# Kernel tuning notes

Hardware: AMD Instinct MI355X
Metric: run time of the kernel (lower is better)

The kernel has to match this reference:

```python
import jax, jax.numpy as jnp
import numpy as np

T, D, H, P, HEADS, EC = 16, 192, 128, 128, 4, 32  # EC = proj_dim // 4
HD = P // HEADS  # head dim = 32


def setup_inputs() -> dict:
    key = jax.random.key(0)
    ks = jax.random.split(key, 16)
    def nrm(k, shp, s=0.02):
        return jax.random.normal(k, shp, jnp.float32) * s
    x = jax.random.normal(ks[0], (T, H, D), jnp.float32)
    u = jax.random.uniform(ks[1], (D, D))
    w = jax.random.uniform(ks[2], (D, D))
    edge_w = jnp.where(u < 0.05, w, 0.0)
    return dict(
        x=x, edge_w=edge_w,
        W_node=nrm(ks[3], (H, P)), b_node=jnp.zeros(P),
        W_edge=nrm(ks[4], (1, EC)), b_edge=jnp.zeros(EC),
        time_enc=nrm(ks[5], (P,)),
        Wqkv=nrm(ks[6], (P, 3 * P)), bqkv=jnp.zeros(3 * P),
        Wo=nrm(ks[7], (P, P)), bo=jnp.zeros(P),
        W1=nrm(ks[8], (P, 4 * P)), b1=jnp.zeros(4 * P),
        W2=nrm(ks[9], (4 * P, P)), b2=jnp.zeros(P),
        g1=jnp.ones(P), beta1=jnp.zeros(P), g2=jnp.ones(P), beta2=jnp.zeros(P),
        Wc1=nrm(ks[10], (2 * P + EC, P)), bc1=jnp.zeros(P),
        Wc2=nrm(ks[11], (P, 1)), bc2=jnp.zeros(1),
        Wd1=nrm(ks[12], (2 * P, P)), bd1=jnp.zeros(P),
        Wd2=nrm(ks[13], (P, 1)), bd2=jnp.zeros(1),
    )


def _ln(z, g, b):
    m = z.mean(-1, keepdims=True)
    v = ((z - m) ** 2).mean(-1, keepdims=True)
    return (z - m) / jnp.sqrt(v + 1e-5) * g + b


def _heads(t, S):
    return t.reshape(S, HEADS, HD).transpose(1, 0, 2)  # (h, S, hd)


def _forward(x, edge_w, W_node, b_node, W_edge, b_edge, time_enc, Wqkv, bqkv,
             Wo, bo, W1, b1, W2, b2, g1, beta1, g2, beta2,
             Wc1, bc1, Wc2, bc2, Wd1, bd1, Wd2, bd2):
    S = T * D
    # node encoder: (T,H,D) -> (T,D,H) -> (T*D,H) -> (T*D,P), dropout is eval-mode identity
    xf = x.transpose(0, 2, 1).reshape(S, H)
    h = jax.nn.relu(xf @ W_node + b_node)
    # learned time encoding scaled by time index
    t_idx = jnp.repeat(jnp.arange(T, dtype=jnp.float32), D)
    h = h + time_enc[None, :] * t_idx[:, None]
    # spatiotemporal mask: attend to self+neighbors at t and t-1 (vectorized kron)
    adj = (edge_w > 0) | jnp.eye(D, dtype=bool)
    time_allow = jnp.eye(T, dtype=bool) | jnp.eye(T, k=-1, dtype=bool)
    allow = (time_allow[:, None, :, None] & adj[None, :, None, :]).reshape(S, S)
    scale = 1.0 / np.sqrt(HD)
    z = h
    for _ in range(2):  # num_layers=2, shared weights as in the source
        y = _ln(z, g1, beta1)
        qkv = y @ Wqkv + bqkv
        q, k, v = jnp.split(qkv, 3, axis=-1)
        scores = jnp.einsum('hqd,hkd->hqk', _heads(q, S), _heads(k, S)) * scale
        scores = jnp.where(allow[None], scores, -jnp.inf)
        a = jax.nn.softmax(scores, axis=-1)
        attn = jnp.einsum('hqk,hkd->hqd', a, _heads(v, S))
        z = z + attn.transpose(1, 0, 2).reshape(S, P) @ Wo + bo
        y = _ln(z, g2, beta2)
        z = z + jax.nn.relu(y @ W1 + b1) @ W2 + b2
    nf = z.reshape(T, D, P)
    curr, nxt = nf[:-1], nf[1:]  # (T-1, D, P)
    # edge encoder: Linear(1->EC)+ReLU on edge weights
    edge_enc = jax.nn.relu(edge_w[:, :, None] * W_edge[0] + b_edge)  # (D, D, EC)
    # update classifier on concat[next_i, curr_j, edge] -> split the first matmul
    hn = nxt @ Wc1[:P]            # (T-1, D, P)
    hc = curr @ Wc1[P:2 * P]      # (T-1, D, P)
    he = edge_enc @ Wc1[2 * P:]   # (D, D, P)
    hcls = jax.nn.relu(hn[:, :, None, :] + hc[:, None, :, :] + he[None] + bc1)
    logits = (hcls @ Wc2)[..., 0] + bc2[0]  # (T-1, D, D)
    mask = (edge_w == 0) & ~jnp.eye(D, dtype=bool)
    logits = jnp.where(mask[None], -1e9, logits)
    # distance predictor on concat[curr, next]
    hd = jax.nn.relu(curr @ Wd1[:P] + nxt @ Wd1[P:] + bd1)
    dist = (hd @ Wd2)[..., 0] + bd2[0]  # (T-1, D)
    return logits, dist


def reference(x, edge_w, W_node, b_node, W_edge, b_edge, time_enc, Wqkv, bqkv,
              Wo, bo, W1, b1, W2, b2, g1, beta1, g2, beta2,
              Wc1, bc1, Wc2, bc2, Wd1, bd1, Wd2, bd2):
    return _forward(x, edge_w, W_node, b_node, W_edge, b_edge, time_enc, Wqkv,
                    bqkv, Wo, bo, W1, b1, W2, b2, g1, beta1, g2, beta2,
                    Wc1, bc1, Wc2, bc2, Wd1, bd1, Wd2, bd2)
```

## Files before the change

kernel.cpp:

```cpp
#include <hip/hip_runtime.h>

constexpr int T_ = 16;
constexpr int D_ = 192;
constexpr int H_ = 128;
constexpr int P_ = 128;
constexpr int EC_ = 32;
constexpr int S_ = T_ * D_;
constexpr int FF_ = 512;
constexpr float SCALE_ = 0.17677669529663687f;

__device__ __forceinline__ float wave_sum64(float v) {
#pragma unroll
  for (int m = 1; m < 64; m <<= 1) v += __shfl_xor(v, m);
  return v;
}

__global__ __launch_bounds__(128) void embed_adj_kernel(
    const float* __restrict__ x, const float* __restrict__ W_node,
    const float* __restrict__ b_node, const float* __restrict__ time_enc,
    const float* __restrict__ edge_w, float* __restrict__ z,
    int* __restrict__ adj_cnt, int* __restrict__ adj_list) {
  int bx = blockIdx.x;
  int tid = threadIdx.x;
  if (bx < D_ && tid < 64) {
    int lane = tid, cnt = 0;
    for (int base = 0; base < D_; base += 64) {
      int j = base + lane;
      bool pred = (edge_w[bx * D_ + j] > 0.f) || (j == bx);
      unsigned long long mb = __ballot(pred);
      int ofs = __popcll(mb & ((1ull << lane) - 1ull));
      if (pred) adj_list[bx * D_ + cnt + ofs] = j;
      cnt += __popcll(mb);
    }
    if (lane == 0) adj_cnt[bx] = cnt;
  }
  __shared__ float As[4 * H_];
  int m0 = bx * 4;
  for (int idx = tid; idx < 4 * H_; idx += 128) {
    int r = idx >> 7, h = idx & 127;
    int s = m0 + r, t = s / D_, d = s - t * D_;
    As[idx] = x[(t * H_ + h) * D_ + d];
  }
  __syncthreads();
  int j = tid;
  float acc[4];
  float bj = b_node[j];
#pragma unroll
  for (int r = 0; r < 4; ++r) acc[r] = bj;
  for (int h = 0; h < H_; h += 4) {
    float w0 = W_node[(h + 0) * P_ + j], w1 = W_node[(h + 1) * P_ + j];
    float w2 = W_node[(h + 2) * P_ + j], w3 = W_node[(h + 3) * P_ + j];
#pragma unroll
    for (int r = 0; r < 4; ++r) {
      const float4 a = *reinterpret_cast<const float4*>(&As[r * H_ + h]);
      acc[r] = fmaf(a.x, w0, acc[r]);
      acc[r] = fmaf(a.y, w1, acc[r]);
      acc[r] = fmaf(a.z, w2, acc[r]);
      acc[r] = fmaf(a.w, w3, acc[r]);
    }
  }
  float te = time_enc[j];
#pragma unroll
  for (int r = 0; r < 4; ++r) {
    int s = m0 + r;
    z[(size_t)s * P_ + j] = fmaxf(acc[r], 0.f) + te * (float)(s / D_);
  }
}

__global__ __launch_bounds__(384) void qkv_kernel(
    const float* __restrict__ z, const float* __restrict__ Wqkv,
    const float* __restrict__ bqkv, const float* __restrict__ g,
    const float* __restrict__ b, float* __restrict__ qkvb) {
  constexpr int BM = 4, N = 384;
  int m0 = blockIdx.x * BM;
  int tid = threadIdx.x;
  __shared__ float As[BM * 128];
  {
    float4* As4 = (float4*)As;
    const float4* Z4 = (const float4*)(z + (size_t)m0 * 128);
    if (tid < BM * 32) As4[tid] = Z4[tid];
  }
  __syncthreads();
  {
    int wv = tid >> 6, lane = tid & 63;
    if (wv < BM) {
      int r = wv;
      float v0 = As[r * 128 + lane], v1 = As[r * 128 + 64 + lane];
      float s = wave_sum64(v0 + v1);
      float mean = s * (1.f / 128.f);
      float d0 = v0 - mean, d1 = v1 - mean;
      float q = wave_sum64(d0 * d0 + d1 * d1);
      float inv = 1.f / sqrtf(q * (1.f / 128.f) + 1e-5f);
      As[r * 128 + lane] = d0 * inv * g[lane] + b[lane];
      As[r * 128 + 64 + lane] = d1 * inv * g[lane + 64] + b[lane + 64];
    }
  }
  __syncthreads();
  int col = tid;
  float acc[BM];
  float bc = bqkv[col];
#pragma unroll
  for (int r = 0; r < BM; ++r) acc[r] = bc;
  for (int k = 0; k < 128; k += 4) {
    float b0 = Wqkv[(size_t)(k + 0) * N + col];
    float b1 = Wqkv[(size_t)(k + 1) * N + col];
    float b2 = Wqkv[(size_t)(k + 2) * N + col];
    float b3 = Wqkv[(size_t)(k + 3) * N + col];
#pragma unroll
    for (int r = 0; r < BM; ++r) {
      const float4 a = *(const float4*)&As[r * 128 + k];
      acc[r] = fmaf(a.x, b0, acc[r]);
      acc[r] = fmaf(a.y, b1, acc[r]);
      acc[r] = fmaf(a.z, b2, acc[r]);
      acc[r] = fmaf(a.w, b3, acc[r]);
    }
  }
#pragma unroll
  for (int r = 0; r < BM; ++r) qkvb[(size_t)(m0 + r) * N + col] = acc[r];
}

__global__ __launch_bounds__(128) void attn_wo_kernel(
    const float* __restrict__ qkvb, const int* __restrict__ adj_cnt,
    const int* __restrict__ adj_list, const float* __restrict__ Wo,
    const float* __restrict__ bo, float* __restrict__ z) {
  int s = blockIdx.x;
  int t = s / D_, d1 = s - t * D_;
  int tid = threadIdx.x;
  __shared__ int klist[D_];
  __shared__ float scores[4][2 * D_];
  __shared__ float att[128];

  int nd2 = adj_cnt[d1];
  for (int kd = tid; kd < nd2; kd += 128) klist[kd] = adj_list[d1 * D_ + kd];
  __syncthreads();
  int t0 = (t > 0) ? t - 1 : 0;
  int ntp = (t > 0) ? 2 : 1;
  int nk = nd2 * ntp;

  float q = qkvb[(size_t)s * 384 + tid];
  int h = tid >> 5, dd = tid & 31;

  for (int tp = 0; tp < ntp; ++tp) {
    int tt = t0 + tp;
    int kd = 0;
    for (; kd + 2 <= nd2; kd += 2) {
      int sk0 = tt * D_ + klist[kd];
      int sk1 = tt * D_ + klist[kd + 1];
      float p0 = q * qkvb[(size_t)sk0 * 384 + P_ + tid];
      float p1 = q * qkvb[(size_t)sk1 * 384 + P_ + tid];
#pragma unroll
      for (int m = 1; m < 32; m <<= 1) {
        p0 += __shfl_xor(p0, m);
        p1 += __shfl_xor(p1, m);
      }
      if (dd == 0) {
        scores[h][tp * nd2 + kd] = p0 * SCALE_;
        scores[h][tp * nd2 + kd + 1] = p1 * SCALE_;
      }
    }
    if (kd < nd2) {
      int sk = tt * D_ + klist[kd];
      float p = q * qkvb[(size_t)sk * 384 + P_ + tid];
#pragma unroll
      for (int m = 1; m < 32; m <<= 1) p += __shfl_xor(p, m);
      if (dd == 0) scores[h][tp * nd2 + kd] = p * SCALE_;
    }
  }
  float mx = -1e30f;
  for (int ki = dd; ki < nk; ki += 32) mx = fmaxf(mx, scores[h][ki]);
#pragma unroll
  for (int m = 1; m < 32; m <<= 1) mx = fmaxf(mx, __shfl_xor(mx, m));
  float ssum = 0.f;
  for (int ki = dd; ki < nk; ki += 32) {
    float e = expf(scores[h][ki] - mx);
    scores[h][ki] = e;
    ssum += e;
  }
#pragma unroll
  for (int m = 1; m < 32; m <<= 1) ssum += __shfl_xor(ssum, m);
  float inv = 1.f / ssum;

  float acc = 0.f;
  for (int tp = 0; tp < ntp; ++tp) {
    int tt = t0 + tp;
    int kd = 0;
    for (; kd + 2 <= nd2; kd += 2) {
      float e0 = scores[h][tp * nd2 + kd];
      float e1 = scores[h][tp * nd2 + kd + 1];
      int sk0 = tt * D_ + klist[kd];
      int sk1 = tt * D_ + klist[kd + 1];
      float v0 = qkvb[(size_t)sk0 * 384 + 2 * P_ + tid];
      float v1 = qkvb[(size_t)sk1 * 384 + 2 * P_ + tid];
      acc = fmaf(e0, v0, acc);
      acc = fmaf(e1, v1, acc);
    }
    if (kd < nd2) {
      float e = scores[h][tp * nd2 + kd];
      int sk = tt * D_ + klist[kd];
      acc = fmaf(e, qkvb[(size_t)sk * 384 + 2 * P_ + tid], acc);
    }
  }
  att[tid] = acc * inv;
  __syncthreads();

  int c = tid;
  float p = 0.f;
  for (int k = 0; k < 128; k += 4) {
    const float4 a = *(const float4*)&att[k];
    p = fmaf(a.x, Wo[(size_t)(k + 0) * P_ + c], p);
    p = fmaf(a.y, Wo[(size_t)(k + 1) * P_ + c], p);
    p = fmaf(a.z, Wo[(size_t)(k + 2) * P_ + c], p);
    p = fmaf(a.w, Wo[(size_t)(k + 3) * P_ + c], p);
  }
  z[(size_t)s * P_ + c] += p + bo[c];
}

__global__ __launch_bounds__(256) void ffn_kernel(
    const float* __restrict__ W1, const float* __restrict__ b1,
    const float* __restrict__ W2, const float* __restrict__ b2,
    const float* __restrict__ g, const float* __restrict__ b,
    float* __restrict__ z) {
  constexpr int BM = 4, NT = 256;
  int m0 = blockIdx.x * BM;
  int tid = threadIdx.x;
  __shared__ float As[BM * 128];
  __shared__ float mid[BM * FF_];
  {
    float4* As4 = (float4*)As;
    const float4* Z4 = (const float4*)(z + (size_t)m0 * 128);
    if (tid < BM * 32) As4[tid] = Z4[tid];
  }
  __syncthreads();
  {
    int wv = tid >> 6, lane = tid & 63;
    float v0 = As[wv * 128 + lane], v1 = As[wv * 128 + 64 + lane];
    float s = wave_sum64(v0 + v1);
    float mean = s * (1.f / 128.f);
    float d0 = v0 - mean, d1 = v1 - mean;
    float qv = wave_sum64(d0 * d0 + d1 * d1);
    float inv = 1.f / sqrtf(qv * (1.f / 128.f) + 1e-5f);
    As[wv * 128 + lane] = d0 * inv * g[lane] + b[lane];
    As[wv * 128 + lane + 64] = d1 * inv * g[lane + 64] + b[lane + 64];
  }
  __syncthreads();
  {
    int c0 = 2 * tid;
    float acc0[BM], acc1[BM];
    float bb0 = b1[c0], bb1 = b1[c0 + 1];
#pragma unroll
    for (int r = 0; r < BM; ++r) {
      acc0[r] = bb0;
      acc1[r] = bb1;
    }
    for (int k = 0; k < 128; k += 4) {
      float2 bv0 = *(const float2*)(W1 + (size_t)(k + 0) * FF_ + c0);
      float2 bv1 = *(const float2*)(W1 + (size_t)(k + 1) * FF_ + c0);
      float2 bv2 = *(const float2*)(W1 + (size_t)(k + 2) * FF_ + c0);
      float2 bv3 = *(const float2*)(W1 + (size_t)(k + 3) * FF_ + c0);
#pragma unroll
      for (int r = 0; r < BM; ++r) {
        const float4 a = *(const float4*)&As[r * 128 + k];
        acc0[r] = fmaf(a.x, bv0.x, acc0[r]);
        acc1[r] = fmaf(a.x, bv0.y, acc1[r]);
        acc0[r] = fmaf(a.y, bv1.x, acc0[r]);
        acc1[r] = fmaf(a.y, bv1.y, acc1[r]);
        acc0[r] = fmaf(a.z, bv2.x, acc0[r]);
        acc1[r] = fmaf(a.z, bv2.y, acc1[r]);
        acc0[r] = fmaf(a.w, bv3.x, acc0[r]);
        acc1[r] = fmaf(a.w, bv3.y, acc1[r]);
      }
    }
#pragma unroll
    for (int r = 0; r < BM; ++r) {
      mid[r * FF_ + c0] = fmaxf(acc0[r], 0.f);
      mid[r * FF_ + c0 + 1] = fmaxf(acc1[r], 0.f);
    }
  }
  __syncthreads();
  {
    int rg = tid >> 7, col = tid & 127;
    int r0 = rg * 2;
    float a0 = 0.f, a1 = 0.f;
    for (int k = 0; k < FF_; k += 4) {
      float w0 = W2[(size_t)(k + 0) * P_ + col];
      float w1 = W2[(size_t)(k + 1) * P_ + col];
      float w2 = W2[(size_t)(k + 2) * P_ + col];
      float w3 = W2[(size_t)(k + 3) * P_ + col];
      const float4 m0v = *(const float4*)&mid[r0 * FF_ + k];
      const float4 m1v = *(const float4*)&mid[(r0 + 1) * FF_ + k];
      a0 = fmaf(m0v.x, w0, a0); a0 = fmaf(m0v.y, w1, a0);
      a0 = fmaf(m0v.z, w2, a0); a0 = fmaf(m0v.w, w3, a0);
      a1 = fmaf(m1v.x, w0, a1); a1 = fmaf(m1v.y, w1, a1);
      a1 = fmaf(m1v.z, w2, a1); a1 = fmaf(m1v.w, w3, a1);
    }
    float bb = b2[col];
    z[(size_t)(m0 + r0) * P_ + col] += a0 + bb;
    z[(size_t)(m0 + r0 + 1) * P_ + col] += a1 + bb;
  }
}

__global__ __launch_bounds__(512) void pre_gemm_kernel(
    const float* __restrict__ A, const float* __restrict__ Wc1,
    const float* __restrict__ Wd1, float* __restrict__ pre) {
  constexpr int K = 128, BM = 8;
  int m0 = blockIdx.x * BM;
  int tid = threadIdx.x;
  __shared__ float As[BM * K];
  {
    float4* As4 = (float4*)As;
    const float4* A4 = (const float4*)(A + (size_t)m0 * K);
    if (tid < 256) As4[tid] = A4[tid];
  }
  __syncthreads();
  int col = tid;
  int seg = col >> 7, cc = col & 127;
  const float* Bbase = (seg < 2 ? Wc1 : Wd1) + ((seg & 1) ? P_ * P_ : 0) + cc;
  float acc[BM];
#pragma unroll
  for (int r = 0; r < BM; ++r) acc[r] = 0.f;
  for (int k = 0; k < K; k += 4) {
    float b0 = Bbase[(size_t)(k + 0) * P_];
    float b1 = Bbase[(size_t)(k + 1) * P_];
    float b2 = Bbase[(size_t)(k + 2) * P_];
    float b3 = Bbase[(size_t)(k + 3) * P_];
#pragma unroll
    for (int r = 0; r < BM; ++r) {
      const float4 a = *(const float4*)&As[r * K + k];
      acc[r] = fmaf(a.x, b0, acc[r]);
      acc[r] = fmaf(a.y, b1, acc[r]);
      acc[r] = fmaf(a.z, b2, acc[r]);
      acc[r] = fmaf(a.w, b3, acc[r]);
    }
  }
#pragma unroll
  for (int r = 0; r < BM; ++r) pre[(size_t)(m0 + r) * 512 + col] = acc[r];
}

__global__ __launch_bounds__(64) void logits_dist_kernel(
    const float* __restrict__ pre, const int* __restrict__ adj_cnt,
    const int* __restrict__ adj_list, const float* __restrict__ edge_w,
    const float* __restrict__ W_edge, const float* __restrict__ b_edge,
    const float* __restrict__ Wc1e, const float* __restrict__ bc1,
    const float* __restrict__ Wc2, const float* __restrict__ bc2,
    const float* __restrict__ bd1, const float* __restrict__ Wd2,
    const float* __restrict__ bd2, float* __restrict__ logits,
    float* __restrict__ dist) {
  int i = blockIdx.x;
  int t = blockIdx.y;
  int lane = threadIdx.x;
  int w = t * D_ + i;
  float* lrow = logits + (size_t)w * D_;
  for (int j = lane; j < D_; j += 64) lrow[j] = -1e9f;

  const float* hnr = pre + (size_t)((t + 1) * D_ + i) * 512;
  float hn0 = hnr[lane], hn1 = hnr[lane + 64];
  float bc1_0 = bc1[lane], bc1_1 = bc1[lane + 64];
  float wc0 = Wc2[lane], wc1 = Wc2[lane + 64];
  float bb = bc2[0];
  int cnt = adj_cnt[i];
  for (int jj = 0; jj < cnt; ++jj) {
    int j = adj_list[i * D_ + jj];
    float wv = edge_w[i * D_ + j];
    float he0 = 0.f, he1 = 0.f;
#pragma unroll 8
    for (int e = 0; e < EC_; ++e) {
      float enc = fmaxf(fmaf(wv, W_edge[e], b_edge[e]), 0.f);
      he0 = fmaf(enc, Wc1e[e * P_ + lane], he0);
      he1 = fmaf(enc, Wc1e[e * P_ + lane + 64], he1);
    }
    const float* hcr = pre + (size_t)(t * D_ + j) * 512 + 128;
    float sacc = fmaxf(hn0 + hcr[lane] + he0 + bc1_0, 0.f) * wc0 +
                 fmaxf(hn1 + hcr[lane + 64] + he1 + bc1_1, 0.f) * wc1;
    sacc = wave_sum64(sacc);
    if (lane == 0) lrow[j] = sacc + bb;
  }

  const float* ar = pre + (size_t)w * 512 + 256;
  const float* br = pre + (size_t)(w + D_) * 512 + 384;
  float v0 = fmaxf(ar[lane] + br[lane] + bd1[lane], 0.f) * Wd2[lane];
  float v1 = fmaxf(ar[lane + 64] + br[lane + 64] + bd1[lane + 64], 0.f) * Wd2[lane + 64];
  float sd = wave_sum64(v0 + v1);
  if (lane == 0) dist[w] = sd + bd2[0];
}

extern "C" void kernel_launch(void* const* d_in, const int* in_sizes, int n_in,
                              void* d_out, int out_size, void* d_ws,
                              size_t ws_size, hipStream_t stream) {
  const float* x = (const float*)d_in[0];
  const float* edge_w = (const float*)d_in[1];
  const float* W_node = (const float*)d_in[2];
  const float* b_node = (const float*)d_in[3];
  const float* W_edge = (const float*)d_in[4];
  const float* b_edge = (const float*)d_in[5];
  const float* time_enc = (const float*)d_in[6];
  const float* Wqkv = (const float*)d_in[7];
  const float* bqkv = (const float*)d_in[8];
  const float* Wo = (const float*)d_in[9];
  const float* bo = (const float*)d_in[10];
  const float* W1 = (const float*)d_in[11];
  const float* b1 = (const float*)d_in[12];
  const float* W2 = (const float*)d_in[13];
  const float* b2 = (const float*)d_in[14];
  const float* g1 = (const float*)d_in[15];
  const float* beta1 = (const float*)d_in[16];
  const float* g2 = (const float*)d_in[17];
  const float* beta2 = (const float*)d_in[18];
  const float* Wc1 = (const float*)d_in[19];
  const float* bc1 = (const float*)d_in[20];
  const float* Wc2 = (const float*)d_in[21];
  const float* bc2 = (const float*)d_in[22];
  const float* Wd1 = (const float*)d_in[23];
  const float* bd1 = (const float*)d_in[24];
  const float* Wd2 = (const float*)d_in[25];
  const float* bd2 = (const float*)d_in[26];

  float* ws = (float*)d_ws;
  float* z = ws;
  float* qkvb = z + S_ * 128;
  float* pre = qkvb + S_ * 384;
  int* adj_cnt = (int*)(pre + S_ * 512);
  int* adj_list = adj_cnt + D_;

  float* logits = (float*)d_out;
  float* dist = (float*)d_out + (T_ - 1) * D_ * D_;

  embed_adj_kernel<<<S_ / 4, 128, 0, stream>>>(x, W_node, b_node, time_enc,
                                               edge_w, z, adj_cnt, adj_list);
  for (int it = 0; it < 2; ++it) {
    qkv_kernel<<<S_ / 4, 384, 0, stream>>>(z, Wqkv, bqkv, g1, beta1, qkvb);
    attn_wo_kernel<<<S_, 128, 0, stream>>>(qkvb, adj_cnt, adj_list, Wo, bo, z);
    ffn_kernel<<<S_ / 4, 256, 0, stream>>>(W1, b1, W2, b2, g2, beta2, z);
  }
  pre_gemm_kernel<<<S_ / 8, 512, 0, stream>>>(z, Wc1, Wd1, pre);
  logits_dist_kernel<<<dim3(D_, T_ - 1), 64, 0, stream>>>(
      pre, adj_cnt, adj_list, edge_w, W_edge, b_edge, Wc1 + 2 * P_ * P_, bc1,
      Wc2, bc2, bd1, Wd2, bd2, logits, dist);
}
```

Before: 295.4 us.

## Fuse embed with first QKV, and FFN with next QKV or final pre-GEMM

Folds the node embedding and the first LayerNorm+QKV projection into one kernel working on 6 rows per block. Each FFN launch now also does the following QKV projection (first layer) or the classifier/distance pre-GEMM (last layer), using the residual rows already in shared memory. This cuts the launch count from 9 to 6 and removes global round trips of z between stages. The cost is larger blocks (512 threads) and fewer rows per block in some GEMMs, so weight reuse per block changes.

```diff
diff --git a/kernel.cpp b/kernel.cpp
--- a/kernel.cpp
+++ b/kernel.cpp
@@ -15,11 +15,15 @@
   return v;
 }
 
-__global__ __launch_bounds__(128) void embed_adj_kernel(
+__global__ __launch_bounds__(384) void embed_qkv_kernel(
     const float* __restrict__ x, const float* __restrict__ W_node,
     const float* __restrict__ b_node, const float* __restrict__ time_enc,
-    const float* __restrict__ edge_w, float* __restrict__ z,
-    int* __restrict__ adj_cnt, int* __restrict__ adj_list) {
+    const float* __restrict__ edge_w, const float* __restrict__ Wqkv,
+    const float* __restrict__ bqkv, const float* __restrict__ g1,
+    const float* __restrict__ beta1, float* __restrict__ z,
+    float* __restrict__ qkvb, int* __restrict__ adj_cnt,
+    int* __restrict__ adj_list) {
+  constexpr int BM = 6;
   int bx = blockIdx.x;
   int tid = threadIdx.x;
   if (bx < D_ && tid < 64) {
@@ -34,89 +38,73 @@
     }
     if (lane == 0) adj_cnt[bx] = cnt;
   }
-  __shared__ float As[4 * H_];
-  int m0 = bx * 4;
-  for (int idx = tid; idx < 4 * H_; idx += 128) {
+  __shared__ float As[BM * 128];
+  __shared__ float zs[BM * 128];
+  int m0 = bx * BM;
+  for (int idx = tid; idx < BM * 128; idx += 384) {
     int r = idx >> 7, h = idx & 127;
     int s = m0 + r, t = s / D_, d = s - t * D_;
     As[idx] = x[(t * H_ + h) * D_ + d];
   }
   __syncthreads();
-  int j = tid;
-  float acc[4];
-  float bj = b_node[j];
-#pragma unroll
-  for (int r = 0; r < 4; ++r) acc[r] = bj;
-  for (int h = 0; h < H_; h += 4) {
-    float w0 = W_node[(h + 0) * P_ + j], w1 = W_node[(h + 1) * P_ + j];
-    float w2 = W_node[(h + 2) * P_ + j], w3 = W_node[(h + 3) * P_ + j];
-#pragma unroll
-    for (int r = 0; r < 4; ++r) {
-      const float4 a = *reinterpret_cast<const float4*>(&As[r * H_ + h]);
-      acc[r] = fmaf(a.x, w0, acc[r]);
-      acc[r] = fmaf(a.y, w1, acc[r]);
-      acc[r] = fmaf(a.z, w2, acc[r]);
-      acc[r] = fmaf(a.w, w3, acc[r]);
-    }
-  }
-  float te = time_enc[j];
-#pragma unroll
-  for (int r = 0; r < 4; ++r) {
-    int s = m0 + r;
-    z[(size_t)s * P_ + j] = fmaxf(acc[r], 0.f) + te * (float)(s / D_);
-  }
-}
-
-__global__ __launch_bounds__(384) void qkv_kernel(
-    const float* __restrict__ z, const float* __restrict__ Wqkv,
-    const float* __restrict__ bqkv, const float* __restrict__ g,
-    const float* __restrict__ b, float* __restrict__ qkvb) {
-  constexpr int BM = 4, N = 384;
-  int m0 = blockIdx.x * BM;
-  int tid = threadIdx.x;
-  __shared__ float As[BM * 128];
-  {
-    float4* As4 = (float4*)As;
-    const float4* Z4 = (const float4*)(z + (size_t)m0 * 128);
-    if (tid < BM * 32) As4[tid] = Z4[tid];
+  {
+    int rg = tid >> 7, col = tid & 127, r0 = rg * 2;
+    float acc0 = b_node[col], acc1 = acc0;
+    for (int h = 0; h < H_; h += 4) {
+      float w0 = W_node[(h + 0) * P_ + col], w1 = W_node[(h + 1) * P_ + col];
+      float w2 = W_node[(h + 2) * P_ + col], w3 = W_node[(h + 3) * P_ + col];
+      const float4 a0 = *(const float4*)&As[r0 * 128 + h];
+      const float4 a1 = *(const float4*)&As[(r0 + 1) * 128 + h];
+      acc0 = fmaf(a0.x, w0, acc0); acc0 = fmaf(a0.y, w1, acc0);
+      acc0 = fmaf(a0.z, w2, acc0); acc0 = fmaf(a0.w, w3, acc0);
+      acc1 = fmaf(a1.x, w0, acc1); acc1 = fmaf(a1.y, w1, acc1);
+      acc1 = fmaf(a1.z, w2, acc1); acc1 = fmaf(a1.w, w3, acc1);
+    }
+    float te = time_enc[col];
+    int s0 = m0 + r0;
+    float v0 = fmaxf(acc0, 0.f) + te * (float)(s0 / D_);
+    float v1 = fmaxf(acc1, 0.f) + te * (float)((s0 + 1) / D_);
+    zs[r0 * 128 + col] = v0;
+    zs[(r0 + 1) * 128 + col] = v1;
+    z[(size_t)s0 * P_ + col] = v0;
+    z[(size_t)(s0 + 1) * P_ + col] = v1;
   }
   __syncthreads();
   {
     int wv = tid >> 6, lane = tid & 63;
-    if (wv < BM) {
-      int r = wv;
-      float v0 = As[r * 128 + lane], v1 = As[r * 128 + 64 + lane];
-      float s = wave_sum64(v0 + v1);
-      float mean = s * (1.f / 128.f);
-      float d0 = v0 - mean, d1 = v1 - mean;
-      float q = wave_sum64(d0 * d0 + d1 * d1);
-      float inv = 1.f / sqrtf(q * (1.f / 128.f) + 1e-5f);
-      As[r * 128 + lane] = d0 * inv * g[lane] + b[lane];
-      As[r * 128 + 64 + lane] = d1 * inv * g[lane + 64] + b[lane + 64];
-    }
-  }
-  __syncthreads();
-  int col = tid;
-  float acc[BM];
-  float bc = bqkv[col];
-#pragma unroll
-  for (int r = 0; r < BM; ++r) acc[r] = bc;
-  for (int k = 0; k < 128; k += 4) {
-    float b0 = Wqkv[(size_t)(k + 0) * N + col];
-    float b1 = Wqkv[(size_t)(k + 1) * N + col];
-    float b2 = Wqkv[(size_t)(k + 2) * N + col];
-    float b3 = Wqkv[(size_t)(k + 3) * N + col];
-#pragma unroll
-    for (int r = 0; r < BM; ++r) {
-      const float4 a = *(const float4*)&As[r * 128 + k];
-      acc[r] = fmaf(a.x, b0, acc[r]);
-      acc[r] = fmaf(a.y, b1, acc[r]);
-      acc[r] = fmaf(a.z, b2, acc[r]);
-      acc[r] = fmaf(a.w, b3, acc[r]);
-    }
-  }
-#pragma unroll
-  for (int r = 0; r < BM; ++r) qkvb[(size_t)(m0 + r) * N + col] = acc[r];
+    float v0 = zs[wv * 128 + lane], v1 = zs[wv * 128 + 64 + lane];
+    float s = wave_sum64(v0 + v1);
+    float mean = s * (1.f / 128.f);
+    float d0 = v0 - mean, d1 = v1 - mean;
+    float q = wave_sum64(d0 * d0 + d1 * d1);
+    float inv = 1.f / sqrtf(q * (1.f / 128.f) + 1e-5f);
+    As[wv * 128 + lane] = d0 * inv * g1[lane] + beta1[lane];
+    As[wv * 128 + 64 + lane] = d1 * inv * g1[lane + 64] + beta1[lane + 64];
+  }
+  __syncthreads();
+  {
+    int col = tid;
+    float acc[BM];
+    float bc = bqkv[col];
+#pragma unroll
+    for (int r = 0; r < BM; ++r) acc[r] = bc;
+    for (int k = 0; k < 128; k += 4) {
+      float b0 = Wqkv[(size_t)(k + 0) * 384 + col];
+      float b1 = Wqkv[(size_t)(k + 1) * 384 + col];
+      float b2 = Wqkv[(size_t)(k + 2) * 384 + col];
+      float b3 = Wqkv[(size_t)(k + 3) * 384 + col];
+#pragma unroll
+      for (int r = 0; r < BM; ++r) {
+        const float4 a = *(const float4*)&As[r * 128 + k];
+        acc[r] = fmaf(a.x, b0, acc[r]);
+        acc[r] = fmaf(a.y, b1, acc[r]);
+        acc[r] = fmaf(a.z, b2, acc[r]);
+        acc[r] = fmaf(a.w, b3, acc[r]);
+      }
+    }
+#pragma unroll
+    for (int r = 0; r < BM; ++r) qkvb[(size_t)(m0 + r) * 384 + col] = acc[r];
+  }
 }
 
 __global__ __launch_bounds__(128) void attn_wo_kernel(
@@ -215,125 +203,142 @@
   z[(size_t)s * P_ + c] += p + bo[c];
 }
 
-__global__ __launch_bounds__(256) void ffn_kernel(
+template <bool NEXT_QKV>
+__global__ __launch_bounds__(512) void ffn_next_kernel(
     const float* __restrict__ W1, const float* __restrict__ b1,
     const float* __restrict__ W2, const float* __restrict__ b2,
-    const float* __restrict__ g, const float* __restrict__ b,
-    float* __restrict__ z) {
-  constexpr int BM = 4, NT = 256;
+    const float* __restrict__ g2, const float* __restrict__ beta2,
+    const float* __restrict__ Wqkv, const float* __restrict__ bqkv,
+    const float* __restrict__ g1, const float* __restrict__ beta1,
+    const float* __restrict__ Wc1, const float* __restrict__ Wd1,
+    float* __restrict__ z, float* __restrict__ qkvb, float* __restrict__ pre) {
+  constexpr int BM = 4;
   int m0 = blockIdx.x * BM;
   int tid = threadIdx.x;
   __shared__ float As[BM * 128];
+  __shared__ float ys[BM * 128];
   __shared__ float mid[BM * FF_];
-  {
-    float4* As4 = (float4*)As;
-    const float4* Z4 = (const float4*)(z + (size_t)m0 * 128);
-    if (tid < BM * 32) As4[tid] = Z4[tid];
-  }
+  if (tid < BM * 32)
+    ((float4*)As)[tid] = ((const float4*)(z + (size_t)m0 * 128))[tid];
   __syncthreads();
   {
     int wv = tid >> 6, lane = tid & 63;
-    float v0 = As[wv * 128 + lane], v1 = As[wv * 128 + 64 + lane];
-    float s = wave_sum64(v0 + v1);
-    float mean = s * (1.f / 128.f);
-    float d0 = v0 - mean, d1 = v1 - mean;
-    float qv = wave_sum64(d0 * d0 + d1 * d1);
-    float inv = 1.f / sqrtf(qv * (1.f / 128.f) + 1e-5f);
-    As[wv * 128 + lane] = d0 * inv * g[lane] + b[lane];
-    As[wv * 128 + lane + 64] = d1 * inv * g[lane + 64] + b[lane + 64];
-  }
-  __syncthreads();
-  {
-    int c0 = 2 * tid;
-    float acc0[BM], acc1[BM];
-    float bb0 = b1[c0], bb1 = b1[c0 + 1];
-#pragma unroll
-    for (int r = 0; r < BM; ++r) {
-      acc0[r] = bb0;
-      acc1[r] = bb1;
-    }
+    if (wv < BM) {
+      float v0 = As[wv * 128 + lane], v1 = As[wv * 128 + 64 + lane];
+      float s = wave_sum64(v0 + v1);
+      float mean = s * (1.f / 128.f);
+      float d0 = v0 - mean, d1 = v1 - mean;
+      float q = wave_sum64(d0 * d0 + d1 * d1);
+      float inv = 1.f / sqrtf(q * (1.f / 128.f) + 1e-5f);
+      ys[wv * 128 + lane] = d0 * inv * g2[lane] + beta2[lane];
+      ys[wv * 128 + 64 + lane] = d1 * inv * g2[lane + 64] + beta2[lane + 64];
+    }
+  }
+  __syncthreads();
+  {
+    int col = tid;
+    float acc[BM];
+    float bb = b1[col];
+#pragma unroll
+    for (int r = 0; r < BM; ++r) acc[r] = bb;
     for (int k = 0; k < 128; k += 4) {
-      float2 bv0 = *(const float2*)(W1 + (size_t)(k + 0) * FF_ + c0);
-      float2 bv1 = *(const float2*)(W1 + (size_t)(k + 1) * FF_ + c0);
-      float2 bv2 = *(const float2*)(W1 + (size_t)(k + 2) * FF_ + c0);
-      float2 bv3 = *(const float2*)(W1 + (size_t)(k + 3) * FF_ + c0);
+      float w0 = W1[(size_t)(k + 0) * FF_ + col];
+      float w1 = W1[(size_t)(k + 1) * FF_ + col];
+      float w2 = W1[(size_t)(k + 2) * FF_ + col];
+      float w3 = W1[(size_t)(k + 3) * FF_ + col];
 #pragma unroll
       for (int r = 0; r < BM; ++r) {
-        const float4 a = *(const float4*)&As[r * 128 + k];
-        acc0[r] = fmaf(a.x, bv0.x, acc0[r]);
-        acc1[r] = fmaf(a.x, bv0.y, acc1[r]);
-        acc0[r] = fmaf(a.y, bv1.x, acc0[r]);
-        acc1[r] = fmaf(a.y, bv1.y, acc1[r]);
-        acc0[r] = fmaf(a.z, bv2.x, acc0[r]);
-        acc1[r] = fmaf(a.z, bv2.y, acc1[r]);
-        acc0[r] = fmaf(a.w, bv3.x, acc0[r]);
-        acc1[r] = fmaf(a.w, bv3.y, acc1[r]);
-      }
-    }
-#pragma unroll
-    for (int r = 0; r < BM; ++r) {
-      mid[r * FF_ + c0] = fmaxf(acc0[r], 0.f);
-      mid[r * FF_ + c0 + 1] = fmaxf(acc1[r], 0.f);
-    }
+        const float4 a = *(const float4*)&ys[r * 128 + k];
+        acc[r] = fmaf(a.x, w0, acc[r]);
+        acc[r] = fmaf(a.y, w1, acc[r]);
+        acc[r] = fmaf(a.z, w2, acc[r]);
+        acc[r] = fmaf(a.w, w3, acc[r]);
+      }
+    }
+#pragma unroll
+    for (int r = 0; r < BM; ++r) mid[r * FF_ + col] = fmaxf(acc[r], 0.f);
   }
   __syncthreads();
   {
     int rg = tid >> 7, col = tid & 127;
-    int r0 = rg * 2;
-    float a0 = 0.f, a1 = 0.f;
+    float a0 = 0.f;
     for (int k = 0; k < FF_; k += 4) {
       float w0 = W2[(size_t)(k + 0) * P_ + col];
       float w1 = W2[(size_t)(k + 1) * P_ + col];
       float w2 = W2[(size_t)(k + 2) * P_ + col];
       float w3 = W2[(size_t)(k + 3) * P_ + col];
-      const float4 m0v = *(const float4*)&mid[r0 * FF_ + k];
-      const float4 m1v = *(const float4*)&mid[(r0 + 1) * FF_ + k];
+      const float4 m0v = *(const float4*)&mid[rg * FF_ + k];
       a0 = fmaf(m0v.x, w0, a0); a0 = fmaf(m0v.y, w1, a0);
       a0 = fmaf(m0v.z, w2, a0); a0 = fmaf(m0v.w, w3, a0);
-      a1 = fmaf(m1v.x, w0, a1); a1 = fmaf(m1v.y, w1, a1);
-      a1 = fmaf(m1v.z, w2, a1); a1 = fmaf(m1v.w, w3, a1);
-    }
-    float bb = b2[col];
-    z[(size_t)(m0 + r0) * P_ + col] += a0 + bb;
-    z[(size_t)(m0 + r0 + 1) * P_ + col] += a1 + bb;
-  }
-}
-
-__global__ __launch_bounds__(512) void pre_gemm_kernel(
-    const float* __restrict__ A, const float* __restrict__ Wc1,
-    const float* __restrict__ Wd1, float* __restrict__ pre) {
-  constexpr int K = 128, BM = 8;
-  int m0 = blockIdx.x * BM;
-  int tid = threadIdx.x;
-  __shared__ float As[BM * K];
-  {
-    float4* As4 = (float4*)As;
-    const float4* A4 = (const float4*)(A + (size_t)m0 * K);
-    if (tid < 256) As4[tid] = A4[tid];
-  }
-  __syncthreads();
-  int col = tid;
-  int seg = col >> 7, cc = col & 127;
-  const float* Bbase = (seg < 2 ? Wc1 : Wd1) + ((seg & 1) ? P_ * P_ : 0) + cc;
-  float acc[BM];
-#pragma unroll
-  for (int r = 0; r < BM; ++r) acc[r] = 0.f;
-  for (int k = 0; k < K; k += 4) {
-    float b0 = Bbase[(size_t)(k + 0) * P_];
-    float b1 = Bbase[(size_t)(k + 1) * P_];
-    float b2 = Bbase[(size_t)(k + 2) * P_];
-    float b3 = Bbase[(size_t)(k + 3) * P_];
-#pragma unroll
-    for (int r = 0; r < BM; ++r) {
-      const float4 a = *(const float4*)&As[r * K + k];
-      acc[r] = fmaf(a.x, b0, acc[r]);
-      acc[r] = fmaf(a.y, b1, acc[r]);
-      acc[r] = fmaf(a.z, b2, acc[r]);
-      acc[r] = fmaf(a.w, b3, acc[r]);
-    }
-  }
-#pragma unroll
-  for (int r = 0; r < BM; ++r) pre[(size_t)(m0 + r) * 512 + col] = acc[r];
+    }
+    float nz = As[rg * 128 + col] + a0 + b2[col];
+    __syncthreads();
+    ys[rg * 128 + col] = nz;
+    if (NEXT_QKV) z[(size_t)(m0 + rg) * P_ + col] = nz;
+  }
+  __syncthreads();
+  if constexpr (NEXT_QKV) {
+    {
+      int wv = tid >> 6, lane = tid & 63;
+      if (wv < BM) {
+        float v0 = ys[wv * 128 + lane], v1 = ys[wv * 128 + 64 + lane];
+        float s = wave_sum64(v0 + v1);
+        float mean = s * (1.f / 128.f);
+        float d0 = v0 - mean, d1 = v1 - mean;
+        float q = wave_sum64(d0 * d0 + d1 * d1);
+        float inv = 1.f / sqrtf(q * (1.f / 128.f) + 1e-5f);
+        As[wv * 128 + lane] = d0 * inv * g1[lane] + beta1[lane];
+        As[wv * 128 + 64 + lane] = d1 * inv * g1[lane + 64] + beta1[lane + 64];
+      }
+    }
+    __syncthreads();
+    if (tid < 384) {
+      int col = tid;
+      float acc[BM];
+      float bc = bqkv[col];
+#pragma unroll
+      for (int r = 0; r < BM; ++r) acc[r] = bc;
+      for (int k = 0; k < 128; k += 4) {
+        float b0 = Wqkv[(size_t)(k + 0) * 384 + col];
+        float b1 = Wqkv[(size_t)(k + 1) * 384 + col];
+        float b2c = Wqkv[(size_t)(k + 2) * 384 + col];
+        float b3 = Wqkv[(size_t)(k + 3) * 384 + col];
+#pragma unroll
+        for (int r = 0; r < BM; ++r) {
+          const float4 a = *(const float4*)&As[r * 128 + k];
+          acc[r] = fmaf(a.x, b0, acc[r]);
+          acc[r] = fmaf(a.y, b1, acc[r]);
+          acc[r] = fmaf(a.z, b2c, acc[r]);
+          acc[r] = fmaf(a.w, b3, acc[r]);
+        }
+      }
+#pragma unroll
+      for (int r = 0; r < BM; ++r) qkvb[(size_t)(m0 + r) * 384 + col] = acc[r];
+    }
+  } else {
+    int col = tid;
+    int seg = col >> 7, cc = col & 127;
+    const float* Bbase = (seg < 2 ? Wc1 : Wd1) + ((seg & 1) ? P_ * P_ : 0) + cc;
+    float acc[BM];
+#pragma unroll
+    for (int r = 0; r < BM; ++r) acc[r] = 0.f;
+    for (int k = 0; k < 128; k += 4) {
+      float b0 = Bbase[(size_t)(k + 0) * P_];
+      float b1 = Bbase[(size_t)(k + 1) * P_];
+      float b2c = Bbase[(size_t)(k + 2) * P_];
+      float b3 = Bbase[(size_t)(k + 3) * P_];
+#pragma unroll
+      for (int r = 0; r < BM; ++r) {
+        const float4 a = *(const float4*)&ys[r * 128 + k];
+        acc[r] = fmaf(a.x, b0, acc[r]);
+        acc[r] = fmaf(a.y, b1, acc[r]);
+        acc[r] = fmaf(a.z, b2c, acc[r]);
+        acc[r] = fmaf(a.w, b3, acc[r]);
+      }
+    }
+#pragma unroll
+    for (int r = 0; r < BM; ++r) pre[(size_t)(m0 + r) * 512 + col] = acc[r];
+  }
 }
 
 __global__ __launch_bounds__(64) void logits_dist_kernel(
@@ -424,14 +429,17 @@
   float* logits = (float*)d_out;
   float* dist = (float*)d_out + (T_ - 1) * D_ * D_;
 
-  embed_adj_kernel<<<S_ / 4, 128, 0, stream>>>(x, W_node, b_node, time_enc,
-                                               edge_w, z, adj_cnt, adj_list);
-  for (int it = 0; it < 2; ++it) {
-    qkv_kernel<<<S_ / 4, 384, 0, stream>>>(z, Wqkv, bqkv, g1, beta1, qkvb);
-    attn_wo_kernel<<<S_, 128, 0, stream>>>(qkvb, adj_cnt, adj_list, Wo, bo, z);
-    ffn_kernel<<<S_ / 4, 256, 0, stream>>>(W1, b1, W2, b2, g2, beta2, z);
-  }
-  pre_gemm_kernel<<<S_ / 8, 512, 0, stream>>>(z, Wc1, Wd1, pre);
+  embed_qkv_kernel<<<S_ / 6, 384, 0, stream>>>(
+      x, W_node, b_node, time_enc, edge_w, Wqkv, bqkv, g1, beta1, z, qkvb,
+      adj_cnt, adj_list);
+  attn_wo_kernel<<<S_, 128, 0, stream>>>(qkvb, adj_cnt, adj_list, Wo, bo, z);
+  ffn_next_kernel<true><<<S_ / 4, 512, 0, stream>>>(
+      W1, b1, W2, b2, g2, beta2, Wqkv, bqkv, g1, beta1, nullptr, nullptr, z,
+      qkvb, nullptr);
+  attn_wo_kernel<<<S_, 128, 0, stream>>>(qkvb, adj_cnt, adj_list, Wo, bo, z);
+  ffn_next_kernel<false><<<S_ / 4, 512, 0, stream>>>(
+      W1, b1, W2, b2, g2, beta2, nullptr, nullptr, nullptr, nullptr, Wc1, Wd1,
+      z, nullptr, pre);
   logits_dist_kernel<<<dim3(D_, T_ - 1), 64, 0, stream>>>(
       pre, adj_cnt, adj_list, edge_w, W_edge, b_edge, Wc1 + 2 * P_ * P_, bc1,
       Wc2, bc2, bd1, Wd2, bd2, logits, dist);
```

Result: slower. 302.8 us (+2.5%).
